# Kernel optimization log

Measured on AMD Instinct MI355X. Metric: run time of the kernel, lower is better.

The kernel has to match this reference:

```python
import jax, jax.numpy as jnp
import numpy as np

B, T, D = 4, 2048, 1024
GROUPS = 32
EPS = 1e-5
THETA = 10000.0


def _rope(x):
    # lucidrains RotaryEmbedding: interleaved pairs over the full dim
    d = x.shape[-1]
    t = x.shape[-2]
    inv_freq = 1.0 / (THETA ** (jnp.arange(0, d, 2, dtype=jnp.float32) / d))  # [d/2]
    freqs = jnp.arange(t, dtype=jnp.float32)[:, None] * inv_freq[None, :]      # [T, d/2]
    cos = jnp.cos(freqs).astype(x.dtype)
    sin = jnp.sin(freqs).astype(x.dtype)
    x1 = x[..., 0::2]
    x2 = x[..., 1::2]
    r1 = x1 * cos - x2 * sin
    r2 = x1 * sin + x2 * cos
    return jnp.stack([r1, r2], axis=-1).reshape(x.shape)


def _group_norm(z, weight, bias):
    # z: [N, C]; normalize per group of C//GROUPS channels
    n, c = z.shape
    zg = z.reshape(n, GROUPS, c // GROUPS)
    mean = zg.mean(axis=-1, keepdims=True)
    var = zg.var(axis=-1, keepdims=True)
    zg = (zg - mean) * jax.lax.rsqrt(var + EPS)
    return zg.reshape(n, c) * weight + bias


def setup_inputs() -> dict:
    key = jax.random.key(0)
    k1, k2, k3 = jax.random.split(key, 3)
    x = jax.random.normal(k1, (B, T, D), dtype=jnp.float32)
    W_in = jax.random.normal(k2, (D, 3 * D), dtype=jnp.float32) * (1.0 / np.sqrt(D))
    b_in = jax.random.normal(k3, (3 * D,), dtype=jnp.float32) * 0.02
    gn_weight = jnp.ones((D,), dtype=jnp.float32)
    gn_bias = jnp.zeros((D,), dtype=jnp.float32)
    return {"x": x, "W_in": W_in, "b_in": b_in, "gn_weight": gn_weight, "gn_bias": gn_bias}


def reference(x, W_in, b_in, gn_weight, gn_bias):
    b, t, c = x.shape
    qkv = x @ W_in + b_in                    # [B,T,3D]
    Q, K, V = jnp.split(qkv, 3, axis=-1)
    Q = jax.nn.relu(_rope(Q))
    K = jax.nn.relu(_rope(K))
    V = jax.nn.relu(V)
    A = jnp.einsum('btd,bsd->bts', Q, K)     # [B,T,T], no softmax
    y = jnp.einsum('bts,bsd->btd', A, V)     # [B,T,D]
    y = _group_norm(y.reshape(-1, c), gn_weight, gn_bias).reshape(b, t, c)
    # faithful to original: transpose(-2,-1).reshape(B,T,dim)
    return jnp.swapaxes(y, -2, -1).reshape(b, t, c)
```

## Files before the change

kernel.cpp:

```cpp
#include <hip/hip_runtime.h>


typedef unsigned short u16;
typedef __attribute__((ext_vector_type(8))) unsigned short u16x8;
typedef __attribute__((ext_vector_type(4))) float fx4;
typedef __attribute__((ext_vector_type(8))) __bf16 bfx8;

#define TP 129

__device__ __forceinline__ u16 f2bh(float v) {
  unsigned u = __float_as_uint(v);
  return (u16)((u + 0x7FFFu + ((u >> 16) & 1u)) >> 16);
}
__device__ __forceinline__ fx4 mfma16(bfx8 a, bfx8 b, fx4 c) {
  return __builtin_amdgcn_mfma_f32_16x16x32_bf16(a, b, c, 0, 0, 0);
}

__device__ __forceinline__ void gload16(const u16* g, u16* l) {
  __builtin_amdgcn_global_load_lds(
      (const __attribute__((address_space(1))) unsigned int*)(const void*)g,
      (__attribute__((address_space(3))) unsigned int*)(void*)l, 16, 0, 0);
}

__device__ __forceinline__ bfx8 ldsw(const u16* lds, int row, int slot) {
  const char* p = (const char*)lds + row * 128 + ((slot ^ (row & 7)) << 4);
  return __builtin_bit_cast(bfx8, *reinterpret_cast<const u16x8*>(p));
}

__device__ __forceinline__ void stage4(const u16* __restrict__ A,
                                       size_t rowBase, int stride, int k0,
                                       u16* lds, int w, int lane) {
#pragma unroll
  for (int i = 0; i < 4; ++i) {
    int c = ((w * 4 + i) << 6) + lane;
    int r = c >> 3, s = c & 7;
    int t = s ^ (r & 7);
    const u16* src = A + (rowBase + (size_t)r) * (size_t)stride + k0 + (t << 3);
    gload16(src, lds + ((w * 4 + i) << 9));
  }
}

__device__ __forceinline__ void stageA2(const u16* __restrict__ A,
                                        size_t rowBase, int stride, int k0,
                                        u16* lds, int w, int lane) {
#pragma unroll
  for (int i = 0; i < 2; ++i) {
    int c = ((w * 2 + i) << 6) + lane;
    int r = c >> 3, s = c & 7;
    int t = s ^ (r & 7);
    const u16* src = A + (rowBase + (size_t)r) * (size_t)stride + k0 + (t << 3);
    gload16(src, lds + ((w * 2 + i) << 9));
  }
}

__device__ inline void gemm_core_pipe(const u16* __restrict__ A, size_t aBase, int aStr,
                                      const u16* __restrict__ B, size_t bBase, int bStr, int K,
                                      u16* sA0, u16* sB0, u16* sA1, u16* sB1,
                                      fx4 acc[4][4], int w, int lane) {
  int wm = (w >> 1) * 64, wn = (w & 1) * 64;
  int lr = lane & 15, lk = lane >> 4;
  stage4(A, aBase, aStr, 0, sA0, w, lane);
  stage4(B, bBase, bStr, 0, sB0, w, lane);
  int NT = K >> 6;
  for (int t = 0; t < NT; ++t) {
    u16* cA = (t & 1) ? sA1 : sA0;
    u16* cB = (t & 1) ? sB1 : sB0;
    if (t + 1 < NT) {
      u16* nA = (t & 1) ? sA0 : sA1;
      u16* nB = (t & 1) ? sB0 : sB1;
      stage4(A, aBase, aStr, (t + 1) << 6, nA, w, lane);
      stage4(B, bBase, bStr, (t + 1) << 6, nB, w, lane);
      asm volatile("s_waitcnt vmcnt(8)" ::: "memory");
    } else {
      asm volatile("s_waitcnt vmcnt(0)" ::: "memory");
    }
    __builtin_amdgcn_s_barrier();
    __builtin_amdgcn_sched_barrier(0);
    bfx8 a[8], b[8];
#pragma unroll
    for (int h = 0; h < 2; ++h)
#pragma unroll
      for (int i = 0; i < 4; ++i) {
        a[h * 4 + i] = ldsw(cA, wm + i * 16 + lr, h * 4 + lk);
        b[h * 4 + i] = ldsw(cB, wn + i * 16 + lr, h * 4 + lk);
      }
    asm volatile("s_waitcnt lgkmcnt(0)" ::: "memory");
    __builtin_amdgcn_sched_barrier(0);
    __builtin_amdgcn_s_barrier();
#pragma unroll
    for (int h = 0; h < 2; ++h)
#pragma unroll
      for (int mi = 0; mi < 4; ++mi)
#pragma unroll
        for (int ni = 0; ni < 4; ++ni)
          acc[mi][ni] = mfma16(a[h * 4 + mi], b[h * 4 + ni], acc[mi][ni]);
  }
}

__global__ void k_prep(const float* __restrict__ x, const float* __restrict__ W,
                       u16* __restrict__ xh, u16* __restrict__ WTh,
                       float2* __restrict__ tabTI, float2* __restrict__ tabIT) {
  __shared__ float tile[32][33];
  int bid = blockIdx.x, tid = threadIdx.x;
  if (bid < 4096) {
    size_t i = ((size_t)bid * 256 + tid) * 8;
    fx4 v0 = *reinterpret_cast<const fx4*>(x + i);
    fx4 v1 = *reinterpret_cast<const fx4*>(x + i + 4);
    u16x8 h;
#pragma unroll
    for (int j = 0; j < 4; ++j) {
      h[j] = f2bh(v0[j]);
      h[4 + j] = f2bh(v1[j]);
    }
    *reinterpret_cast<u16x8*>(xh + i) = h;
  } else if (bid < 7168) {
    int idx = bid - 4096;
    int n0 = (idx % 96) * 32, k0 = (idx / 96) * 32;
    int c = tid & 31, r4 = tid >> 5;
#pragma unroll
    for (int it = 0; it < 4; ++it) {
      int r = r4 + it * 8;
      tile[r][c] = W[(size_t)(k0 + r) * 3072 + n0 + c];
    }
    __syncthreads();
#pragma unroll
    for (int it = 0; it < 4; ++it) {
      int r = r4 + it * 8;
      WTh[(size_t)(n0 + r) * 1024 + k0 + c] = f2bh(tile[c][r]);
    }
  } else {
    int half = (bid - 7168) >> 12;
    int idx = ((bid - 7168) & 4095) * 256 + tid;
    int t, i;
    if (half == 0) {
      t = idx >> 9;
      i = idx & 511;
    } else {
      i = idx >> 11;
      t = idx & 2047;
    }
    float invf = exp2f(-(float)i * (13.287712379549449f / 512.f));
    float ang = (float)t * invf, s, c;
    sincosf(ang, &s, &c);
    if (half == 0)
      tabTI[idx] = make_float2(c, s);
    else
      tabIT[idx] = make_float2(c, s);
  }
}

__global__ __launch_bounds__(256) void k_gemm1f(const u16* __restrict__ xh,
                                                const u16* __restrict__ WTh,
                                                const float* __restrict__ b_in,
                                                const float2* __restrict__ tabTI,
                                                const float2* __restrict__ tabIT,
                                                u16* __restrict__ Qh, u16* __restrict__ Kth,
                                                u16* __restrict__ Vth) {
  __shared__ __align__(16) char smembuf[81920];
  float* shbuf = (float*)smembuf;
  u16* sA0 = (u16*)smembuf;
  u16* sA1 = sA0 + 128 * 64;
  u16* sB0 = sA1 + 128 * 64;
  u16* sB1 = sB0 + 128 * 64;
  u16* sB2 = sB1 + 128 * 64;
  int bid = blockIdx.x;
  int xcd = bid & 7, idx = bid >> 3;
  int mt = (xcd << 3) + (idx & 7), nt = idx >> 3;
  int m0 = mt << 7, n0 = nt << 7;
  int tid = threadIdx.x, lane = tid & 63, w = tid >> 6;
  int wm = (w >> 1) * 64, wn = (w & 1) * 64;
  int lr = lane & 15, lk = lane >> 4;
  fx4 acc[4][4];
#pragma unroll
  for (int i = 0; i < 4; ++i)
#pragma unroll
    for (int j = 0; j < 4; ++j) acc[i][j] = fx4{0.f, 0.f, 0.f, 0.f};

  stage4(xh, (size_t)m0, 1024, 0, sA0, w, lane);
  stage4(WTh, (size_t)n0, 1024, 0, sB0, w, lane);
  stage4(WTh, (size_t)n0, 1024, 64, sB1, w, lane);
  const int NT = 16;
  for (int t = 0; t < NT; ++t) {
    u16* cA = (t & 1) ? sA1 : sA0;
    int bm = t % 3;
    u16* cB = (bm == 0) ? sB0 : (bm == 1) ? sB1 : sB2;
    if (t + 2 < NT) {
      u16* nA = (t & 1) ? sA0 : sA1;
      int b2 = (t + 2) % 3;
      u16* nB = (b2 == 0) ? sB0 : (b2 == 1) ? sB1 : sB2;
      stage4(xh, (size_t)m0, 1024, (t + 1) << 6, nA, w, lane);
      stage4(WTh, (size_t)n0, 1024, (t + 2) << 6, nB, w, lane);
      asm volatile("s_waitcnt vmcnt(12)" ::: "memory");
    } else if (t + 1 < NT) {
      u16* nA = (t & 1) ? sA0 : sA1;
      stage4(xh, (size_t)m0, 1024, (t + 1) << 6, nA, w, lane);
      asm volatile("s_waitcnt vmcnt(8)" ::: "memory");
    } else {
      asm volatile("s_waitcnt vmcnt(0)" ::: "memory");
    }
    __builtin_amdgcn_s_barrier();
    __builtin_amdgcn_sched_barrier(0);
    bfx8 a[8], b[8];
#pragma unroll
    for (int h = 0; h < 2; ++h)
#pragma unroll
      for (int i = 0; i < 4; ++i) {
        a[h * 4 + i] = ldsw(cA, wm + i * 16 + lr, h * 4 + lk);
        b[h * 4 + i] = ldsw(cB, wn + i * 16 + lr, h * 4 + lk);
      }
    asm volatile("s_waitcnt lgkmcnt(0)" ::: "memory");
    __builtin_amdgcn_sched_barrier(0);
    __builtin_amdgcn_s_barrier();
#pragma unroll
    for (int h = 0; h < 2; ++h)
#pragma unroll
      for (int mi = 0; mi < 4; ++mi)
#pragma unroll
        for (int ni = 0; ni < 4; ++ni)
          acc[mi][ni] = mfma16(a[h * 4 + mi], b[h * 4 + ni], acc[mi][ni]);
  }

  float bv[4];
#pragma unroll
  for (int ni = 0; ni < 4; ++ni) bv[ni] = b_in[n0 + wn + ni * 16 + lr];
  __syncthreads();
#pragma unroll
  for (int mi = 0; mi < 4; ++mi)
#pragma unroll
    for (int ni = 0; ni < 4; ++ni)
#pragma unroll
      for (int r = 0; r < 4; ++r)
        shbuf[(wn + ni * 16 + lr) * TP + wm + mi * 16 + lk * 4 + r] = acc[mi][ni][r] + bv[ni];
  __syncthreads();

  int part = n0 >> 10;
  int d0 = n0 - (part << 10);
  int bb = m0 >> 11, tb = m0 & 2047;
  int rl0 = tid >> 4;
  int cc = (tid & 15) * 8;

  if (part == 2) {
#pragma unroll
    for (int pass = 0; pass < 8; ++pass) {
      int rl = rl0 + pass * 16;
      u16x8 o;
#pragma unroll
      for (int j = 0; j < 8; ++j) o[j] = f2bh(fmaxf(shbuf[rl * TP + cc + j], 0.f));
      *reinterpret_cast<u16x8*>(Vth + (((size_t)(bb << 10) + d0 + rl) << 11) + tb + cc) = o;
    }
  } else if (part == 1) {
#pragma unroll
    for (int pass = 0; pass < 8; ++pass) {
      int rl = rl0 + pass * 16;
      int d = d0 + rl;
      const float2* tp = tabIT + ((size_t)(d >> 1) << 11) + tb + cc;
      const float* e = shbuf + (rl & ~1) * TP + cc;
      const float* oo = shbuf + (rl | 1) * TP + cc;
      int isOdd = d & 1;
      u16x8 o;
#pragma unroll
      for (int j = 0; j < 8; ++j) {
        float2 cs = tp[j];
        float x1 = e[j], x2 = oo[j];
        float v = isOdd ? (x1 * cs.y + x2 * cs.x) : (x1 * cs.x - x2 * cs.y);
        o[j] = f2bh(fmaxf(v, 0.f));
      }
      *reinterpret_cast<u16x8*>(Kth + (((size_t)(bb << 10) + d) << 11) + tb + cc) = o;
    }
  } else {
#pragma unroll
    for (int pass = 0; pass < 8; ++pass) {
      int rl = rl0 + pass * 16;
      int m = m0 + rl, t = m & 2047;
      const float2* tp = tabTI + ((size_t)t << 9) + ((d0 + cc) >> 1);
      u16x8 o;
#pragma unroll
      for (int jp = 0; jp < 4; ++jp) {
        float x1 = shbuf[(cc + 2 * jp) * TP + rl];
        float x2 = shbuf[(cc + 2 * jp + 1) * TP + rl];
        float2 cs = tp[jp];
        o[2 * jp] = f2bh(fmaxf(x1 * cs.x - x2 * cs.y, 0.f));
        o[2 * jp + 1] = f2bh(fmaxf(x1 * cs.y + x2 * cs.x, 0.f));
      }
      *reinterpret_cast<u16x8*>(Qh + ((size_t)m << 10) + d0 + cc) = o;
    }
  }
}

__global__ __launch_bounds__(256) void k_gemm2(const u16* __restrict__ Kth, const u16* __restrict__ Vth,
                                               u16* __restrict__ KtVTh) {
  __shared__ u16 smem[2 * (64 + 128) * 64];
  u16* sA0 = smem;
  u16* sB0 = sA0 + 64 * 64;
  u16* sA1 = sB0 + 128 * 64;
  u16* sB1 = sA1 + 64 * 64;
  fx4 acc[4][2];
#pragma unroll
  for (int i = 0; i < 4; ++i)
#pragma unroll
    for (int j = 0; j < 2; ++j) acc[i][j] = fx4{0.f, 0.f, 0.f, 0.f};
  int bid = blockIdx.x;
  int xcd = bid & 7, idx = bid >> 3;
  int b = xcd >> 1;
  int mt = (xcd & 1) * 8 + (idx & 7), nt = idx >> 3;
  int m0 = mt << 6, n0 = nt << 7;
  int tid = threadIdx.x, lane = tid & 63, w = tid >> 6;
  int wn2 = w * 32;
  int lr = lane & 15, lk = lane >> 4;
  const u16* Ab = Kth + ((size_t)b << 21);
  const u16* Bb = Vth + ((size_t)b << 21);

  stageA2(Ab, (size_t)m0, 2048, 0, sA0, w, lane);
  stage4(Bb, (size_t)n0, 2048, 0, sB0, w, lane);
  const int NT = 32;
  for (int t = 0; t < NT; ++t) {
    u16* cA = (t & 1) ? sA1 : sA0;
    u16* cB = (t & 1) ? sB1 : sB0;
    if (t + 1 < NT) {
      u16* nA = (t & 1) ? sA0 : sA1;
      u16* nB = (t & 1) ? sB0 : sB1;
      stageA2(Ab, (size_t)m0, 2048, (t + 1) << 6, nA, w, lane);
      stage4(Bb, (size_t)n0, 2048, (t + 1) << 6, nB, w, lane);
      asm volatile("s_waitcnt vmcnt(6)" ::: "memory");
    } else {
      asm volatile("s_waitcnt vmcnt(0)" ::: "memory");
    }
    __builtin_amdgcn_s_barrier();
    __builtin_amdgcn_sched_barrier(0);
    bfx8 a[8], bfr[4];
#pragma unroll
    for (int h = 0; h < 2; ++h) {
#pragma unroll
      for (int i = 0; i < 4; ++i) a[h * 4 + i] = ldsw(cA, i * 16 + lr, h * 4 + lk);
#pragma unroll
      for (int j = 0; j < 2; ++j) bfr[h * 2 + j] = ldsw(cB, wn2 + j * 16 + lr, h * 4 + lk);
    }
    asm volatile("s_waitcnt lgkmcnt(0)" ::: "memory");
    __builtin_amdgcn_sched_barrier(0);
    __builtin_amdgcn_s_barrier();
#pragma unroll
    for (int h = 0; h < 2; ++h)
#pragma unroll
      for (int mi = 0; mi < 4; ++mi)
#pragma unroll
        for (int ni = 0; ni < 2; ++ni)
          acc[mi][ni] = mfma16(a[h * 4 + mi], bfr[h * 2 + ni], acc[mi][ni]);
  }
#pragma unroll
  for (int mi = 0; mi < 4; ++mi)
#pragma unroll
    for (int ni = 0; ni < 2; ++ni)
#pragma unroll
      for (int r = 0; r < 4; ++r) {
        int m = m0 + mi * 16 + lk * 4 + r;
        int n = n0 + wn2 + ni * 16 + lr;
        KtVTh[((size_t)b << 20) + ((size_t)n << 10) + m] = f2bh(acc[mi][ni][r]);
      }
}

__global__ __launch_bounds__(256) void k_gemm3g(const u16* __restrict__ Qh, const u16* __restrict__ KtVTh,
                                                const float* __restrict__ gw, const float* __restrict__ gb,
                                                float* __restrict__ out) {
  __shared__ u16 smem[4 * 128 * 64];
  u16* sA0 = smem;
  u16* sB0 = sA0 + 128 * 64;
  u16* sA1 = sB0 + 128 * 64;
  u16* sB1 = sA1 + 128 * 64;
  fx4 acc[4][4];
#pragma unroll
  for (int i = 0; i < 4; ++i)
#pragma unroll
    for (int j = 0; j < 4; ++j) acc[i][j] = fx4{0.f, 0.f, 0.f, 0.f};
  int bid = blockIdx.x;
  int xcd = bid & 7, idx = bid >> 3;
  int b = xcd >> 1;
  int mt = (xcd & 1) * 8 + (idx & 7), nt = idx >> 3;
  int m0 = mt << 7, n0 = nt << 7;
  int tid = threadIdx.x, lane = tid & 63, w = tid >> 6;
  gemm_core_pipe(Qh, (size_t)(b * 2048 + m0), 1024, KtVTh + ((size_t)b << 20), (size_t)n0, 1024,
                 1024, sA0, sB0, sA1, sB1, acc, w, lane);
  int wm = (w >> 1) * 64, wn = (w & 1) * 64, lr = lane & 15, lk = lane >> 4;
  float wv[4], bvv[4];
#pragma unroll
  for (int ni = 0; ni < 4; ++ni) {
    int n = n0 + wn + ni * 16 + lr;
    wv[ni] = gw[n];
    bvv[ni] = gb[n];
  }
#pragma unroll
  for (int mi = 0; mi < 4; ++mi) {
    fx4 o0, o1, o2, o3;
#pragma unroll
    for (int r = 0; r < 4; ++r) {
      float v0 = acc[mi][0][r], v1 = acc[mi][1][r], v2 = acc[mi][2][r], v3 = acc[mi][3][r];
      float sA2 = v0 + v1, sB2 = v2 + v3;
#pragma unroll
      for (int mk = 1; mk <= 8; mk <<= 1) {
        sA2 += __shfl_xor(sA2, mk);
        sB2 += __shfl_xor(sB2, mk);
      }
      float mA = sA2 * (1.f / 32.f), mB = sB2 * (1.f / 32.f);
      float dA = (v0 - mA) * (v0 - mA) + (v1 - mA) * (v1 - mA);
      float dB = (v2 - mB) * (v2 - mB) + (v3 - mB) * (v3 - mB);
#pragma unroll
      for (int mk = 1; mk <= 8; mk <<= 1) {
        dA += __shfl_xor(dA, mk);
        dB += __shfl_xor(dB, mk);
      }
      float rA = rsqrtf(dA * (1.f / 32.f) + 1e-5f);
      float rB = rsqrtf(dB * (1.f / 32.f) + 1e-5f);
      o0[r] = (v0 - mA) * rA * wv[0] + bvv[0];
      o1[r] = (v1 - mA) * rA * wv[1] + bvv[1];
      o2[r] = (v2 - mB) * rB * wv[2] + bvv[2];
      o3[r] = (v3 - mB) * rB * wv[3] + bvv[3];
    }
    int mbase = m0 + wm + mi * 16 + lk * 4;
#pragma unroll
    for (int ni = 0; ni < 4; ++ni) {
      int n = n0 + wn + ni * 16 + lr;
      fx4 ov = (ni == 0) ? o0 : (ni == 1) ? o1 : (ni == 2) ? o2 : o3;
      *reinterpret_cast<fx4*>(out + (((size_t)(b << 10) + n) << 11) + mbase) = ov;
    }
  }
}

extern "C" void kernel_launch(void* const* d_in, const int* in_sizes, int n_in,
                              void* d_out, int out_size, void* d_ws, size_t ws_size,
                              hipStream_t stream) {
  const float* x = (const float*)d_in[0];
  const float* W = (const float*)d_in[1];
  const float* b_in = (const float*)d_in[2];
  const float* gnw = (const float*)d_in[3];
  const float* gnb = (const float*)d_in[4];
  float* out = (float*)d_out;
  char* ws = (char*)d_ws;

  u16* xh = (u16*)(ws + 0);
  u16* WTh = (u16*)(ws + 16777216);
  u16* Qh = (u16*)(ws + 23068672);
  u16* Kth = (u16*)(ws + 39845888);
  u16* Vth = (u16*)(ws + 56623104);
  u16* KtVTh = (u16*)(ws + 73400320);
  float2* tabTI = (float2*)(ws + 81788928);
  float2* tabIT = (float2*)(ws + 90177536);

  k_prep<<<15360, 256, 0, stream>>>(x, W, xh, WTh, tabTI, tabIT);
  k_gemm1f<<<1536, 256, 0, stream>>>(xh, WTh, b_in, tabTI, tabIT, Qh, Kth, Vth);
  k_gemm2<<<512, 256, 0, stream>>>(Kth, Vth, KtVTh);
  k_gemm3g<<<512, 256, 0, stream>>>(Qh, KtVTh, gnw, gnb, out);
}
```

Baseline: 133.7 us.

## Enlarge QKV GEMM tiles to 256x256 with 512-thread blocks

The first GEMM kernel moves from 128x128 tiles with 256 threads to 256x256 tiles with 512 threads. Each wave now computes 128x64, and staging drops from triple-buffered B to plain double buffering. The epilogue stages the float tile through shared memory in four 64-column quarters with barriers, because the full tile no longer fits. The goal is more operand reuse per global load. The cost is 384 blocks, fewer than two waves over the CUs, one block per CU because of 128KB of LDS, and a serialized epilogue.

```diff
diff --git a/kernel.cpp b/kernel.cpp
--- a/kernel.cpp
+++ b/kernel.cpp
@@ -7,6 +7,7 @@
 typedef __attribute__((ext_vector_type(8))) __bf16 bfx8;
 
 #define TP 129
+#define FP 261
 
 __device__ __forceinline__ u16 f2bh(float v) {
   unsigned u = __float_as_uint(v);
@@ -149,141 +150,140 @@
   }
 }
 
-__global__ __launch_bounds__(256) void k_gemm1f(const u16* __restrict__ xh,
+__global__ __launch_bounds__(512) void k_gemm1f(const u16* __restrict__ xh,
                                                 const u16* __restrict__ WTh,
                                                 const float* __restrict__ b_in,
                                                 const float2* __restrict__ tabTI,
                                                 const float2* __restrict__ tabIT,
                                                 u16* __restrict__ Qh, u16* __restrict__ Kth,
                                                 u16* __restrict__ Vth) {
-  __shared__ __align__(16) char smembuf[81920];
-  float* shbuf = (float*)smembuf;
-  u16* sA0 = (u16*)smembuf;
-  u16* sA1 = sA0 + 128 * 64;
-  u16* sB0 = sA1 + 128 * 64;
-  u16* sB1 = sB0 + 128 * 64;
-  u16* sB2 = sB1 + 128 * 64;
+  __shared__ __align__(16) u16 smem[65536];
+  u16* sA0 = smem;
+  u16* sB0 = smem + 16384;
+  u16* sA1 = smem + 32768;
+  u16* sB1 = smem + 49152;
   int bid = blockIdx.x;
   int xcd = bid & 7, idx = bid >> 3;
-  int mt = (xcd << 3) + (idx & 7), nt = idx >> 3;
-  int m0 = mt << 7, n0 = nt << 7;
+  int mt = (xcd << 2) + (idx & 3), nt = idx >> 2;
+  int m0 = mt << 8, n0 = nt << 8;
   int tid = threadIdx.x, lane = tid & 63, w = tid >> 6;
-  int wm = (w >> 1) * 64, wn = (w & 1) * 64;
+  int wm2 = (w >> 2) << 7, wn2 = (w & 3) << 6;
   int lr = lane & 15, lk = lane >> 4;
-  fx4 acc[4][4];
-#pragma unroll
-  for (int i = 0; i < 4; ++i)
+  fx4 acc[8][4];
+#pragma unroll
+  for (int i = 0; i < 8; ++i)
 #pragma unroll
     for (int j = 0; j < 4; ++j) acc[i][j] = fx4{0.f, 0.f, 0.f, 0.f};
 
   stage4(xh, (size_t)m0, 1024, 0, sA0, w, lane);
   stage4(WTh, (size_t)n0, 1024, 0, sB0, w, lane);
-  stage4(WTh, (size_t)n0, 1024, 64, sB1, w, lane);
   const int NT = 16;
   for (int t = 0; t < NT; ++t) {
     u16* cA = (t & 1) ? sA1 : sA0;
-    int bm = t % 3;
-    u16* cB = (bm == 0) ? sB0 : (bm == 1) ? sB1 : sB2;
-    if (t + 2 < NT) {
+    u16* cB = (t & 1) ? sB1 : sB0;
+    if (t + 1 < NT) {
       u16* nA = (t & 1) ? sA0 : sA1;
-      int b2 = (t + 2) % 3;
-      u16* nB = (b2 == 0) ? sB0 : (b2 == 1) ? sB1 : sB2;
+      u16* nB = (t & 1) ? sB0 : sB1;
       stage4(xh, (size_t)m0, 1024, (t + 1) << 6, nA, w, lane);
-      stage4(WTh, (size_t)n0, 1024, (t + 2) << 6, nB, w, lane);
-      asm volatile("s_waitcnt vmcnt(12)" ::: "memory");
-    } else if (t + 1 < NT) {
-      u16* nA = (t & 1) ? sA0 : sA1;
-      stage4(xh, (size_t)m0, 1024, (t + 1) << 6, nA, w, lane);
+      stage4(WTh, (size_t)n0, 1024, (t + 1) << 6, nB, w, lane);
       asm volatile("s_waitcnt vmcnt(8)" ::: "memory");
     } else {
       asm volatile("s_waitcnt vmcnt(0)" ::: "memory");
     }
     __builtin_amdgcn_s_barrier();
     __builtin_amdgcn_sched_barrier(0);
-    bfx8 a[8], b[8];
-#pragma unroll
-    for (int h = 0; h < 2; ++h)
-#pragma unroll
-      for (int i = 0; i < 4; ++i) {
-        a[h * 4 + i] = ldsw(cA, wm + i * 16 + lr, h * 4 + lk);
-        b[h * 4 + i] = ldsw(cB, wn + i * 16 + lr, h * 4 + lk);
-      }
+    bfx8 a[2][8], b[2][4];
+#pragma unroll
+    for (int kh = 0; kh < 2; ++kh) {
+#pragma unroll
+      for (int mi = 0; mi < 8; ++mi) a[kh][mi] = ldsw(cA, wm2 + mi * 16 + lr, kh * 4 + lk);
+#pragma unroll
+      for (int ni = 0; ni < 4; ++ni) b[kh][ni] = ldsw(cB, wn2 + ni * 16 + lr, kh * 4 + lk);
+    }
     asm volatile("s_waitcnt lgkmcnt(0)" ::: "memory");
     __builtin_amdgcn_sched_barrier(0);
     __builtin_amdgcn_s_barrier();
 #pragma unroll
-    for (int h = 0; h < 2; ++h)
-#pragma unroll
-      for (int mi = 0; mi < 4; ++mi)
+    for (int kh = 0; kh < 2; ++kh)
+#pragma unroll
+      for (int mi = 0; mi < 8; ++mi)
 #pragma unroll
         for (int ni = 0; ni < 4; ++ni)
-          acc[mi][ni] = mfma16(a[h * 4 + mi], b[h * 4 + ni], acc[mi][ni]);
-  }
-
-  float bv[4];
-#pragma unroll
-  for (int ni = 0; ni < 4; ++ni) bv[ni] = b_in[n0 + wn + ni * 16 + lr];
+          acc[mi][ni] = mfma16(a[kh][mi], b[kh][ni], acc[mi][ni]);
+  }
   __syncthreads();
-#pragma unroll
-  for (int mi = 0; mi < 4; ++mi)
-#pragma unroll
-    for (int ni = 0; ni < 4; ++ni)
-#pragma unroll
-      for (int r = 0; r < 4; ++r)
-        shbuf[(wn + ni * 16 + lr) * TP + wm + mi * 16 + lk * 4 + r] = acc[mi][ni][r] + bv[ni];
-  __syncthreads();
-
+
+  float* ftile = (float*)smem;
   int part = n0 >> 10;
   int d0 = n0 - (part << 10);
   int bb = m0 >> 11, tb = m0 & 2047;
-  int rl0 = tid >> 4;
-  int cc = (tid & 15) * 8;
-
-  if (part == 2) {
-#pragma unroll
-    for (int pass = 0; pass < 8; ++pass) {
-      int rl = rl0 + pass * 16;
-      u16x8 o;
-#pragma unroll
-      for (int j = 0; j < 8; ++j) o[j] = f2bh(fmaxf(shbuf[rl * TP + cc + j], 0.f));
-      *reinterpret_cast<u16x8*>(Vth + (((size_t)(bb << 10) + d0 + rl) << 11) + tb + cc) = o;
-    }
-  } else if (part == 1) {
-#pragma unroll
-    for (int pass = 0; pass < 8; ++pass) {
-      int rl = rl0 + pass * 16;
-      int d = d0 + rl;
-      const float2* tp = tabIT + ((size_t)(d >> 1) << 11) + tb + cc;
-      const float* e = shbuf + (rl & ~1) * TP + cc;
-      const float* oo = shbuf + (rl | 1) * TP + cc;
-      int isOdd = d & 1;
-      u16x8 o;
-#pragma unroll
-      for (int j = 0; j < 8; ++j) {
-        float2 cs = tp[j];
-        float x1 = e[j], x2 = oo[j];
-        float v = isOdd ? (x1 * cs.y + x2 * cs.x) : (x1 * cs.x - x2 * cs.y);
-        o[j] = f2bh(fmaxf(v, 0.f));
-      }
-      *reinterpret_cast<u16x8*>(Kth + (((size_t)(bb << 10) + d) << 11) + tb + cc) = o;
-    }
-  } else {
-#pragma unroll
-    for (int pass = 0; pass < 8; ++pass) {
-      int rl = rl0 + pass * 16;
-      int m = m0 + rl, t = m & 2047;
-      const float2* tp = tabTI + ((size_t)t << 9) + ((d0 + cc) >> 1);
-      u16x8 o;
-#pragma unroll
-      for (int jp = 0; jp < 4; ++jp) {
-        float x1 = shbuf[(cc + 2 * jp) * TP + rl];
-        float x2 = shbuf[(cc + 2 * jp + 1) * TP + rl];
-        float2 cs = tp[jp];
-        o[2 * jp] = f2bh(fmaxf(x1 * cs.x - x2 * cs.y, 0.f));
-        o[2 * jp + 1] = f2bh(fmaxf(x1 * cs.y + x2 * cs.x, 0.f));
-      }
-      *reinterpret_cast<u16x8*>(Qh + ((size_t)m << 10) + d0 + cc) = o;
-    }
+  float bv[4];
+#pragma unroll
+  for (int ni = 0; ni < 4; ++ni) bv[ni] = b_in[n0 + wn2 + ni * 16 + lr];
+
+#pragma unroll
+  for (int q = 0; q < 4; ++q) {
+    if ((w & 3) == q) {
+#pragma unroll
+      for (int mi = 0; mi < 8; ++mi)
+#pragma unroll
+        for (int ni = 0; ni < 4; ++ni)
+#pragma unroll
+          for (int r = 0; r < 4; ++r)
+            ftile[(ni * 16 + lr) * FP + wm2 + mi * 16 + lk * 4 + r] = acc[mi][ni][r] + bv[ni];
+    }
+    __syncthreads();
+    int dq0 = d0 + (q << 6);
+    if (part == 2) {
+#pragma unroll
+      for (int i2 = 0; i2 < 4; ++i2) {
+        int item = i2 * 512 + tid;
+        int nl = item >> 5, c8 = (item & 31) * 8;
+        u16x8 o;
+#pragma unroll
+        for (int j = 0; j < 8; ++j) o[j] = f2bh(fmaxf(ftile[nl * FP + c8 + j], 0.f));
+        *reinterpret_cast<u16x8*>(Vth + (((size_t)(bb << 10) + dq0 + nl) << 11) + tb + c8) = o;
+      }
+    } else if (part == 1) {
+#pragma unroll
+      for (int i2 = 0; i2 < 4; ++i2) {
+        int item = i2 * 512 + tid;
+        int nl = item >> 5, c8 = (item & 31) * 8;
+        int d = dq0 + nl;
+        const float2* tp = tabIT + ((size_t)(d >> 1) << 11) + tb + c8;
+        const float* e = ftile + (nl & ~1) * FP + c8;
+        const float* oo = ftile + (nl | 1) * FP + c8;
+        int isOdd = d & 1;
+        u16x8 o;
+#pragma unroll
+        for (int j = 0; j < 8; ++j) {
+          float2 cs = tp[j];
+          float x1 = e[j], x2 = oo[j];
+          float v = isOdd ? (x1 * cs.y + x2 * cs.x) : (x1 * cs.x - x2 * cs.y);
+          o[j] = f2bh(fmaxf(v, 0.f));
+        }
+        *reinterpret_cast<u16x8*>(Kth + (((size_t)(bb << 10) + d) << 11) + tb + c8) = o;
+      }
+    } else {
+#pragma unroll
+      for (int i2 = 0; i2 < 4; ++i2) {
+        int item = i2 * 512 + tid;
+        int ml = item >> 3, c16 = (item & 7) * 8;
+        int m = m0 + ml, t = m & 2047;
+        const float2* tp = tabTI + ((size_t)t << 9) + ((dq0 + c16) >> 1);
+        u16x8 o;
+#pragma unroll
+        for (int jp = 0; jp < 4; ++jp) {
+          float x1 = ftile[(c16 + 2 * jp) * FP + ml];
+          float x2 = ftile[(c16 + 2 * jp + 1) * FP + ml];
+          float2 cs = tp[jp];
+          o[2 * jp] = f2bh(fmaxf(x1 * cs.x - x2 * cs.y, 0.f));
+          o[2 * jp + 1] = f2bh(fmaxf(x1 * cs.y + x2 * cs.x, 0.f));
+        }
+        *reinterpret_cast<u16x8*>(Qh + ((size_t)m << 10) + dq0 + c16) = o;
+      }
+    }
+    __syncthreads();
   }
 }
 
@@ -445,7 +445,7 @@
   float2* tabIT = (float2*)(ws + 90177536);
 
   k_prep<<<15360, 256, 0, stream>>>(x, W, xh, WTh, tabTI, tabIT);
-  k_gemm1f<<<1536, 256, 0, stream>>>(xh, WTh, b_in, tabTI, tabIT, Qh, Kth, Vth);
+  k_gemm1f<<<384, 512, 0, stream>>>(xh, WTh, b_in, tabTI, tabIT, Qh, Kth, Vth);
   k_gemm2<<<512, 256, 0, stream>>>(Kth, Vth, KtVTh);
   k_gemm3g<<<512, 256, 0, stream>>>(Qh, KtVTh, gnw, gnb, out);
 }
```

New measurement: 143.0 us. 7.0% more time.
